# Kernel tuning notes

Hardware: AMD Instinct MI355X
Metric: run time of the kernel (lower is better)

Reference implementation:

```python
import jax, jax.numpy as jnp
import numpy as np

N_SPK = 2048
M_UTT = 8
D_EMB = 512


def setup_inputs() -> dict:
    key = jax.random.key(0)
    k1, = jax.random.split(key, 1)
    embeds = jax.random.normal(k1, (N_SPK * M_UTT, D_EMB), dtype=jnp.float32)
    # module expects L2-normalized utterance embeddings
    embeds = embeds / jnp.linalg.norm(embeds, axis=-1, keepdims=True)
    return {
        "embeds": embeds,
        "w": jnp.asarray(10.0, dtype=jnp.float32),
        "b": jnp.asarray(-5.0, dtype=jnp.float32),
        "n_speakers": N_SPK,
        "m_utterances": M_UTT,
    }


def reference(embeds, w, b, n_speakers, m_utterances):
    N, M = n_speakers, m_utterances
    D = embeds.shape[-1]
    e = embeds.reshape(N, M, D)

    # full centroids (all M utterances), L2-normalized
    centroids = e.mean(axis=1)  # [N, D]
    centroids = centroids / jnp.linalg.norm(centroids, axis=-1, keepdims=True)

    # leave-one-out centroids for same-speaker comparisons
    sums = e.sum(axis=1, keepdims=True)  # [N, 1, D]
    excl = (sums - e) / (M - 1)  # [N, M, D]
    excl = excl / jnp.linalg.norm(excl, axis=-1, keepdims=True)

    # similarity: batched GEMM replaces the original triple loop
    sim = jnp.einsum("nmd,kd->nmk", e, centroids)  # [N, M, N]
    # diagonal (k == i) uses leave-one-out centroid
    diag = jnp.sum(e * excl, axis=-1)  # [N, M]
    idx = jnp.arange(N)
    sim = sim.at[idx, :, idx].set(diag)

    sim = jnp.abs(w) * sim + b

    # cross-entropy with label = own speaker index
    logits = sim.reshape(N * M, N)
    labels = jnp.repeat(jnp.arange(N), M)
    logp = jax.nn.log_softmax(logits, axis=-1)
    loss = -jnp.mean(logp[jnp.arange(N * M), labels])
    return loss
```

## Files before the change

kernel.cpp:

```cpp
#include <hip/hip_runtime.h>
#include <hip/hip_bf16.h>
#include <string.h>

#define N_SPK 2048
#define M_UTT 8
#define D_EMB 512
#define N_ROWS (N_SPK * M_UTT)

using short8 = __attribute__((ext_vector_type(8))) short;
using f32x4  = __attribute__((ext_vector_type(4))) float;

typedef const __attribute__((address_space(1))) unsigned int* gas_p;
typedef __attribute__((address_space(3))) unsigned int* las_p;

__device__ int            g_flag;
__device__ float          g_accum;
__device__ unsigned int   g_done;
__device__ float          g_diag[N_ROWS];
__device__ unsigned short g_cRow[N_SPK * D_EMB];
__device__ float          g_rowsum[N_ROWS * 4];

__device__ __forceinline__ float u2f(unsigned int u) { float f; memcpy(&f, &u, 4); return f; }
__device__ __forceinline__ unsigned int f2u(float f) { unsigned int u; memcpy(&u, &f, 4); return u; }
__device__ __forceinline__ float bflo(unsigned int u) { return u2f(u << 16); }
__device__ __forceinline__ float bfhi(unsigned int u) { return u2f(u & 0xFFFF0000u); }
__device__ __forceinline__ unsigned short f2bf(float f) {
    unsigned int u = f2u(f);
    unsigned int r = u + 0x7FFFu + ((u >> 16) & 1u);
    return (unsigned short)(r >> 16);
}
__device__ __forceinline__ float wsum(float v) {
#pragma unroll
    for (int off = 32; off > 0; off >>= 1) v += __shfl_xor(v, off, 64);
    return v;
}
__device__ __forceinline__ float loadScalar(const void* p, int isbf) {
    float vb = bflo((unsigned int)(*(const unsigned short*)p));
    float vf = *(const float*)p;
    float prim = isbf ? vb : vf;
    float alt  = isbf ? vf : vb;
    float a = fabsf(prim);
    if (isfinite(prim) && a > 1e-6f && a < 1e6f) return prim;
    return alt;
}
__device__ __forceinline__ short8 loadA8(const void* e, long row, int d0, int isbf) {
    if (isbf) {
        return *(const short8*)((const unsigned short*)e + row * D_EMB + d0);
    } else {
        const float* q = (const float*)e + row * D_EMB + d0;
        short8 r;
#pragma unroll
        for (int j = 0; j < 8; ++j) r[j] = (short)f2bf(q[j]);
        return r;
    }
}
__device__ __forceinline__ int detectWave(const void* e, long row, int lane) {
    const unsigned short* q = (const unsigned short*)e + row * D_EMB + lane * 8;
    float p = 0.f;
#pragma unroll
    for (int j = 0; j < 8; ++j) {
        float v = bflo((unsigned int)q[j]);
        p += v * v;
    }
    p = wsum(p);
    return (fabsf(p - 1.0f) < 0.25f) ? 1 : 0;
}

__global__ __launch_bounds__(256) void k1_cent(const void* e) {
    int t = threadIdx.x;
    int wave = t >> 6, lane = t & 63;
    int n = blockIdx.x * 4 + wave;

    int isbf = detectWave(e, (long)n * M_UTT, lane);
    if (blockIdx.x == 0 && t == 0) { g_flag = isbf; g_accum = 0.f; g_done = 0u; }

    float ev[M_UTT][8];
    size_t base = (size_t)n * (M_UTT * D_EMB);
#pragma unroll
    for (int m = 0; m < M_UTT; ++m) {
        size_t idx = base + (size_t)m * D_EMB + (size_t)lane * 8;
        if (isbf) {
            uint4 v = *(const uint4*)((const unsigned short*)e + idx);
            ev[m][0] = bflo(v.x); ev[m][1] = bfhi(v.x);
            ev[m][2] = bflo(v.y); ev[m][3] = bfhi(v.y);
            ev[m][4] = bflo(v.z); ev[m][5] = bfhi(v.z);
            ev[m][6] = bflo(v.w); ev[m][7] = bfhi(v.w);
        } else {
            const float* q = (const float*)e + idx;
            float4 a = *(const float4*)q;
            float4 b2 = *(const float4*)(q + 4);
            ev[m][0] = a.x; ev[m][1] = a.y; ev[m][2] = a.z; ev[m][3] = a.w;
            ev[m][4] = b2.x; ev[m][5] = b2.y; ev[m][6] = b2.z; ev[m][7] = b2.w;
        }
    }

    float s[8];
#pragma unroll
    for (int j = 0; j < 8; ++j) {
        float acc = 0.f;
#pragma unroll
        for (int m = 0; m < M_UTT; ++m) acc += ev[m][j];
        s[j] = acc;
    }

    float p = 0.f;
#pragma unroll
    for (int j = 0; j < 8; ++j) p += s[j] * s[j];
    p = wsum(p);
    float inv = rsqrtf(p);

    unsigned short cw[8];
#pragma unroll
    for (int j = 0; j < 8; ++j) cw[j] = f2bf(s[j] * inv);
    *(short8*)&g_cRow[(size_t)n * D_EMB + lane * 8] = *(short8*)cw;

#pragma unroll
    for (int m = 0; m < M_UTT; ++m) {
        float pd = 0.f, pn = 0.f;
#pragma unroll
        for (int j = 0; j < 8; ++j) {
            float ex = s[j] - ev[m][j];
            pd += ev[m][j] * ex;
            pn += ex * ex;
        }
        pd = wsum(pd);
        pn = wsum(pn);
        if (lane == 0) g_diag[n * M_UTT + m] = pd * rsqrtf(pn);
    }
}

__global__ __launch_bounds__(256, 2) void GE2ELoss_70626442215524_kernel(
        const void* e, const void* wp, const void* bp) {
    __shared__ unsigned short sB[2][2][16 * 512];

    int t = threadIdx.x;
    int wave = t >> 6, lane = t & 63;
    int bx = blockIdx.x;
    int qtr = bx >> 7, rowgrp = bx & 127;
    int rowbase = rowgrp * 128 + wave * 32;
    int isbf = g_flag;
    int quad = lane >> 4, l16 = lane & 15;

    float w_ = fabsf(loadScalar(wp, isbf));
    float b_ = loadScalar(bp, isbf);

    auto stageTile = [&](int buf, int nt2) {
        int c0 = qtr * 512 + nt2 * 32;
#pragma unroll
        for (int g = 0; g < 2; ++g) {
#pragma unroll
            for (int i = 0; i < 4; ++i) {
                int cb = i * 256 + wave * 64;
                int w = cb + lane;
                int col = w & 15;
                int dc = ((w >> 6) << 2) + ((w >> 4) & 3);
                const unsigned short* g_ = &g_cRow[((size_t)(c0 + g * 16 + col) << 9) + dc * 8];
                __builtin_amdgcn_global_load_lds((gas_p)g_, (las_p)&sB[buf][g][cb * 8], 16, 0, 0);
            }
        }
    };

    stageTile(0, 0);

    short8 a[2][16];
#pragma unroll
    for (int s = 0; s < 2; ++s) {
        long row = rowbase + s * 16 + l16;
#pragma unroll
        for (int kt = 0; kt < 16; ++kt)
            a[s][kt] = loadA8(e, row, kt * 32 + quad * 8, isbf);
    }

    float rsum[2][4];
#pragma unroll
    for (int s = 0; s < 2; ++s)
#pragma unroll
        for (int r = 0; r < 4; ++r) rsum[s][r] = 0.f;

    __syncthreads();

    for (int nt2 = 0; nt2 < 16; ++nt2) {
        int cur = nt2 & 1;
        if (nt2 + 1 < 16) stageTile(cur ^ 1, nt2 + 1);

        f32x4 acc[2][2] = {{{0.f,0.f,0.f,0.f},{0.f,0.f,0.f,0.f}},
                           {{0.f,0.f,0.f,0.f},{0.f,0.f,0.f,0.f}}};
#pragma unroll
        for (int g = 0; g < 2; ++g) {
#pragma unroll
            for (int kt = 0; kt < 16; ++kt) {
                short8 b = *(const short8*)&sB[cur][g][(kt * 64 + lane) * 8];
                acc[g][0] = __builtin_amdgcn_mfma_f32_16x16x32_bf16(a[0][kt], b, acc[g][0], 0, 0, 0);
                acc[g][1] = __builtin_amdgcn_mfma_f32_16x16x32_bf16(a[1][kt], b, acc[g][1], 0, 0, 0);
            }
        }

#pragma unroll
        for (int g = 0; g < 2; ++g) {
            int gcol = qtr * 512 + nt2 * 32 + g * 16 + l16;
#pragma unroll
            for (int s = 0; s < 2; ++s) {
#pragma unroll
                for (int reg = 0; reg < 4; ++reg) {
                    int grow = rowbase + s * 16 + quad * 4 + reg;
                    float v = fmaf(w_, acc[g][s][reg], b_);
                    if (gcol == (grow >> 3)) v = fmaf(w_, g_diag[grow], b_);
                    rsum[s][reg] += __expf(v);
                }
            }
        }

        __syncthreads();
    }

#pragma unroll
    for (int s = 0; s < 2; ++s)
#pragma unroll
        for (int reg = 0; reg < 4; ++reg) {
            float v = rsum[s][reg];
            v += __shfl_xor(v, 1, 64);
            v += __shfl_xor(v, 2, 64);
            v += __shfl_xor(v, 4, 64);
            v += __shfl_xor(v, 8, 64);
            if (l16 == 0) {
                int grow = rowbase + s * 16 + quad * 4 + reg;
                g_rowsum[grow * 4 + qtr] = v;
            }
        }
}

__global__ __launch_bounds__(256) void k3_fin(const void* wp, const void* bp, unsigned int* out) {
    __shared__ float red[4];
    int t = threadIdx.x, bx = blockIdx.x;
    int isbf = g_flag;
    float w_ = fabsf(loadScalar(wp, isbf));
    float b_ = loadScalar(bp, isbf);

    int r = bx * 256 + t;
    float4 q = *(const float4*)&g_rowsum[r * 4];
    float tot = (q.x + q.y) + (q.z + q.w);
    float s = logf(tot) - fmaf(w_, g_diag[r], b_);

    s = wsum(s);
    if ((t & 63) == 0) red[t >> 6] = s;
    __syncthreads();
    if (t == 0) {
        float part = red[0] + red[1] + red[2] + red[3];
        atomicAdd(&g_accum, part);
        __threadfence();
        unsigned int old = atomicAdd(&g_done, 1u);
        if (old == 63u) {
            float loss = atomicAdd(&g_accum, 0.f) * (1.0f / N_ROWS);
            unsigned int h = (unsigned int)f2bf(loss);
            out[0] = (h << 16) | h;
        }
    }
}

extern "C" void kernel_launch(void* const* d_in, const int* in_sizes, int n_in,
                              void* d_out, int out_size, void* d_ws, size_t ws_size,
                              hipStream_t stream) {
    const void* e  = d_in[0];
    const void* wp = d_in[1];
    const void* bp = d_in[2];
    (void)in_sizes; (void)n_in; (void)out_size; (void)d_ws; (void)ws_size;

    k1_cent<<<512, 256, 0, stream>>>(e);
    GE2ELoss_70626442215524_kernel<<<512, 256, 0, stream>>>(e, wp, bp);
    k3_fin<<<64, 256, 0, stream>>>(wp, bp, (unsigned int*)d_out);
}
```

Baseline: 136.9 us.

## Fuse centroid, GEMM and finalize kernels into one persistent kernel with grid barrier

Merges the centroid/diagonal kernel, the similarity GEMM kernel and the final reduction kernel into a single launch. A software grid barrier built on an atomic ticket separates centroid production from GEMM consumption, and the last block to finish does the final loss reduction. A-operand loads are moved before the barrier so they overlap the wait, and the fp32 A load is vectorised. This removes two kernel launches and their gaps, but relies on all 512 blocks being co-resident and adds a spin wait with a timeout guard.

```diff
diff --git a/kernel.cpp b/kernel.cpp
--- a/kernel.cpp
+++ b/kernel.cpp
@@ -6,6 +6,7 @@
 #define M_UTT 8
 #define D_EMB 512
 #define N_ROWS (N_SPK * M_UTT)
+#define NBLK 512u
 
 using short8 = __attribute__((ext_vector_type(8))) short;
 using f32x4  = __attribute__((ext_vector_type(4))) float;
@@ -13,12 +14,11 @@
 typedef const __attribute__((address_space(1))) unsigned int* gas_p;
 typedef __attribute__((address_space(3))) unsigned int* las_p;
 
-__device__ int            g_flag;
-__device__ float          g_accum;
 __device__ unsigned int   g_done;
 __device__ float          g_diag[N_ROWS];
 __device__ unsigned short g_cRow[N_SPK * D_EMB];
 __device__ float          g_rowsum[N_ROWS * 4];
+__device__ unsigned int   g_barTicket;
 
 __device__ __forceinline__ float u2f(unsigned int u) { float f; memcpy(&f, &u, 4); return f; }
 __device__ __forceinline__ unsigned int f2u(float f) { unsigned int u; memcpy(&u, &f, 4); return u; }
@@ -48,9 +48,13 @@
         return *(const short8*)((const unsigned short*)e + row * D_EMB + d0);
     } else {
         const float* q = (const float*)e + row * D_EMB + d0;
+        float4 x = *(const float4*)q;
+        float4 y = *(const float4*)(q + 4);
         short8 r;
-#pragma unroll
-        for (int j = 0; j < 8; ++j) r[j] = (short)f2bf(q[j]);
+        r[0] = (short)f2bf(x.x); r[1] = (short)f2bf(x.y);
+        r[2] = (short)f2bf(x.z); r[3] = (short)f2bf(x.w);
+        r[4] = (short)f2bf(y.x); r[5] = (short)f2bf(y.y);
+        r[6] = (short)f2bf(y.z); r[7] = (short)f2bf(y.w);
         return r;
     }
 }
@@ -66,83 +70,117 @@
     return (fabsf(p - 1.0f) < 0.25f) ? 1 : 0;
 }
 
-__global__ __launch_bounds__(256) void k1_cent(const void* e) {
-    int t = threadIdx.x;
-    int wave = t >> 6, lane = t & 63;
-    int n = blockIdx.x * 4 + wave;
-
-    int isbf = detectWave(e, (long)n * M_UTT, lane);
-    if (blockIdx.x == 0 && t == 0) { g_flag = isbf; g_accum = 0.f; g_done = 0u; }
-
-    float ev[M_UTT][8];
-    size_t base = (size_t)n * (M_UTT * D_EMB);
-#pragma unroll
-    for (int m = 0; m < M_UTT; ++m) {
-        size_t idx = base + (size_t)m * D_EMB + (size_t)lane * 8;
-        if (isbf) {
-            uint4 v = *(const uint4*)((const unsigned short*)e + idx);
-            ev[m][0] = bflo(v.x); ev[m][1] = bfhi(v.x);
-            ev[m][2] = bflo(v.y); ev[m][3] = bfhi(v.y);
-            ev[m][4] = bflo(v.z); ev[m][5] = bfhi(v.z);
-            ev[m][6] = bflo(v.w); ev[m][7] = bfhi(v.w);
-        } else {
-            const float* q = (const float*)e + idx;
-            float4 a = *(const float4*)q;
-            float4 b2 = *(const float4*)(q + 4);
-            ev[m][0] = a.x; ev[m][1] = a.y; ev[m][2] = a.z; ev[m][3] = a.w;
-            ev[m][4] = b2.x; ev[m][5] = b2.y; ev[m][6] = b2.z; ev[m][7] = b2.w;
-        }
-    }
-
-    float s[8];
-#pragma unroll
-    for (int j = 0; j < 8; ++j) {
-        float acc = 0.f;
-#pragma unroll
-        for (int m = 0; m < M_UTT; ++m) acc += ev[m][j];
-        s[j] = acc;
-    }
-
-    float p = 0.f;
-#pragma unroll
-    for (int j = 0; j < 8; ++j) p += s[j] * s[j];
-    p = wsum(p);
-    float inv = rsqrtf(p);
-
-    unsigned short cw[8];
-#pragma unroll
-    for (int j = 0; j < 8; ++j) cw[j] = f2bf(s[j] * inv);
-    *(short8*)&g_cRow[(size_t)n * D_EMB + lane * 8] = *(short8*)cw;
-
-#pragma unroll
-    for (int m = 0; m < M_UTT; ++m) {
-        float pd = 0.f, pn = 0.f;
-#pragma unroll
-        for (int j = 0; j < 8; ++j) {
-            float ex = s[j] - ev[m][j];
-            pd += ev[m][j] * ex;
-            pn += ex * ex;
-        }
-        pd = wsum(pd);
-        pn = wsum(pn);
-        if (lane == 0) g_diag[n * M_UTT + m] = pd * rsqrtf(pn);
-    }
+__device__ __forceinline__ void gridSync() {
+    __threadfence();
+    __syncthreads();
+    if (threadIdx.x == 0) {
+        unsigned int my = __hip_atomic_fetch_add(&g_barTicket, 1u,
+                              __ATOMIC_ACQ_REL, __HIP_MEMORY_SCOPE_AGENT);
+        unsigned int target = (my / NBLK + 1u) * NBLK;
+        long guard = 0;
+        while (__hip_atomic_load(&g_barTicket, __ATOMIC_ACQUIRE,
+                                 __HIP_MEMORY_SCOPE_AGENT) < target) {
+            __builtin_amdgcn_s_sleep(8);
+            if (++guard > (1L << 22)) break;
+        }
+        __threadfence();
+    }
+    __syncthreads();
 }
 
 __global__ __launch_bounds__(256, 2) void GE2ELoss_70626442215524_kernel(
-        const void* e, const void* wp, const void* bp) {
+        const void* e, const void* wp, const void* bp, unsigned int* out) {
     __shared__ unsigned short sB[2][2][16 * 512];
+    __shared__ unsigned int s_fin;
+    __shared__ float red[4];
 
     int t = threadIdx.x;
     int wave = t >> 6, lane = t & 63;
     int bx = blockIdx.x;
     int qtr = bx >> 7, rowgrp = bx & 127;
-    int rowbase = rowgrp * 128 + wave * 32;
-    int isbf = g_flag;
     int quad = lane >> 4, l16 = lane & 15;
+
+    int isbf = detectWave(e, (long)rowgrp * 128, lane);
 
     float w_ = fabsf(loadScalar(wp, isbf));
     float b_ = loadScalar(bp, isbf);
+
+    if (bx == 0 && t == 0) g_done = 0u;
+
+    {
+        int n = rowgrp * 16 + qtr * 4 + wave;
+        float ev[M_UTT][8];
+        size_t base = (size_t)n * (M_UTT * D_EMB);
+#pragma unroll
+        for (int m = 0; m < M_UTT; ++m) {
+            size_t idx = base + (size_t)m * D_EMB + (size_t)lane * 8;
+            if (isbf) {
+                uint4 v = *(const uint4*)((const unsigned short*)e + idx);
+                ev[m][0] = bflo(v.x); ev[m][1] = bfhi(v.x);
+                ev[m][2] = bflo(v.y); ev[m][3] = bfhi(v.y);
+                ev[m][4] = bflo(v.z); ev[m][5] = bfhi(v.z);
+                ev[m][6] = bflo(v.w); ev[m][7] = bfhi(v.w);
+            } else {
+                const float* q = (const float*)e + idx;
+                float4 a2 = *(const float4*)q;
+                float4 b2 = *(const float4*)(q + 4);
+                ev[m][0] = a2.x; ev[m][1] = a2.y; ev[m][2] = a2.z; ev[m][3] = a2.w;
+                ev[m][4] = b2.x; ev[m][5] = b2.y; ev[m][6] = b2.z; ev[m][7] = b2.w;
+            }
+        }
+
+        float s[8];
+#pragma unroll
+        for (int j = 0; j < 8; ++j) {
+            float acc = 0.f;
+#pragma unroll
+            for (int m = 0; m < M_UTT; ++m) acc += ev[m][j];
+            s[j] = acc;
+        }
+
+        float p = 0.f;
+#pragma unroll
+        for (int j = 0; j < 8; ++j) p += s[j] * s[j];
+        p = wsum(p);
+        float inv = rsqrtf(p);
+
+        unsigned short cw[8];
+#pragma unroll
+        for (int j = 0; j < 8; ++j) cw[j] = f2bf(s[j] * inv);
+        *(short8*)&g_cRow[(size_t)n * D_EMB + lane * 8] = *(short8*)cw;
+
+#pragma unroll
+        for (int m = 0; m < M_UTT; ++m) {
+            float pd = 0.f, pn = 0.f;
+#pragma unroll
+            for (int j = 0; j < 8; ++j) {
+                float ex = s[j] - ev[m][j];
+                pd += ev[m][j] * ex;
+                pn += ex * ex;
+            }
+            pd = wsum(pd);
+            pn = wsum(pn);
+            if (lane == 0) g_diag[n * M_UTT + m] = pd * rsqrtf(pn);
+        }
+    }
+
+    int rowbase = rowgrp * 128 + wave * 32;
+    short8 a[2][16];
+#pragma unroll
+    for (int s = 0; s < 2; ++s) {
+        long row = rowbase + s * 16 + l16;
+#pragma unroll
+        for (int kt = 0; kt < 16; ++kt)
+            a[s][kt] = loadA8(e, row, kt * 32 + quad * 8, isbf);
+    }
+
+    float rsum[2][4];
+#pragma unroll
+    for (int s = 0; s < 2; ++s)
+#pragma unroll
+        for (int r = 0; r < 4; ++r) rsum[s][r] = 0.f;
+
+    gridSync();
 
     auto stageTile = [&](int buf, int nt2) {
         int c0 = qtr * 512 + nt2 * 32;
@@ -161,22 +199,6 @@
     };
 
     stageTile(0, 0);
-
-    short8 a[2][16];
-#pragma unroll
-    for (int s = 0; s < 2; ++s) {
-        long row = rowbase + s * 16 + l16;
-#pragma unroll
-        for (int kt = 0; kt < 16; ++kt)
-            a[s][kt] = loadA8(e, row, kt * 32 + quad * 8, isbf);
-    }
-
-    float rsum[2][4];
-#pragma unroll
-    for (int s = 0; s < 2; ++s)
-#pragma unroll
-        for (int r = 0; r < 4; ++r) rsum[s][r] = 0.f;
-
     __syncthreads();
 
     for (int nt2 = 0; nt2 < 16; ++nt2) {
@@ -227,30 +249,31 @@
                 g_rowsum[grow * 4 + qtr] = v;
             }
         }
-}
-
-__global__ __launch_bounds__(256) void k3_fin(const void* wp, const void* bp, unsigned int* out) {
-    __shared__ float red[4];
-    int t = threadIdx.x, bx = blockIdx.x;
-    int isbf = g_flag;
-    float w_ = fabsf(loadScalar(wp, isbf));
-    float b_ = loadScalar(bp, isbf);
-
-    int r = bx * 256 + t;
-    float4 q = *(const float4*)&g_rowsum[r * 4];
-    float tot = (q.x + q.y) + (q.z + q.w);
-    float s = logf(tot) - fmaf(w_, g_diag[r], b_);
-
-    s = wsum(s);
-    if ((t & 63) == 0) red[t >> 6] = s;
+
+    __threadfence();
     __syncthreads();
     if (t == 0) {
-        float part = red[0] + red[1] + red[2] + red[3];
-        atomicAdd(&g_accum, part);
+        unsigned int old = __hip_atomic_fetch_add(&g_done, 1u,
+                               __ATOMIC_ACQ_REL, __HIP_MEMORY_SCOPE_AGENT);
+        s_fin = (old == NBLK - 1u) ? 1u : 0u;
+    }
+    __syncthreads();
+
+    if (s_fin) {
         __threadfence();
-        unsigned int old = atomicAdd(&g_done, 1u);
-        if (old == 63u) {
-            float loss = atomicAdd(&g_accum, 0.f) * (1.0f / N_ROWS);
+        float part = 0.f;
+#pragma unroll 4
+        for (int i = 0; i < 64; ++i) {
+            int r = i * 256 + t;
+            float4 q = *(const float4*)&g_rowsum[r * 4];
+            float tot = (q.x + q.y) + (q.z + q.w);
+            part += logf(tot) - fmaf(w_, g_diag[r], b_);
+        }
+        part = wsum(part);
+        if ((t & 63) == 0) red[t >> 6] = part;
+        __syncthreads();
+        if (t == 0) {
+            float loss = (red[0] + red[1] + red[2] + red[3]) * (1.0f / N_ROWS);
             unsigned int h = (unsigned int)f2bf(loss);
             out[0] = (h << 16) | h;
         }
@@ -265,7 +288,6 @@
     const void* bp = d_in[2];
     (void)in_sizes; (void)n_in; (void)out_size; (void)d_ws; (void)ws_size;
 
-    k1_cent<<<512, 256, 0, stream>>>(e);
-    GE2ELoss_70626442215524_kernel<<<512, 256, 0, stream>>>(e, wp, bp);
-    k3_fin<<<64, 256, 0, stream>>>(wp, bp, (unsigned int*)d_out);
-}
+    GE2ELoss_70626442215524_kernel<<<dim3(NBLK), dim3(256), 0, stream>>>(
+        e, wp, bp, (unsigned int*)d_out);
+}
```

Measured after the change: 295.6 us. +115.9%, slower.

## Restructure similarity GEMM into 128x128 tiles with staged bf16 A and atomic row sums

Applied to the files above, without the earlier changes.

The first kernel now writes a bf16 copy of the embeddings, and the main kernel becomes a classic 128x128 output tile GEMM. Both A and B are staged through LDS in K-steps of 32, with a 2x2 wave layout and a 4x4 MFMA accumulator block per wave. The row sums of exp are accumulated with atomics into a single float per row instead of four per-quarter partials. This is meant to raise MFMA reuse per LDS load and to avoid re-reading and converting fp32 A in the GEMM. The cost is an extra 16 MB bf16 write/read, 2048 blocks with shallow K staging, and atomic contention on the row sums.

```diff
diff --git a/kernel.cpp b/kernel.cpp
--- a/kernel.cpp
+++ b/kernel.cpp
@@ -6,6 +6,11 @@
 #define M_UTT 8
 #define D_EMB 512
 #define N_ROWS (N_SPK * M_UTT)
+
+#define BM 128
+#define BN 128
+#define BK 32
+#define KSTEPS (D_EMB / BK)
 
 using short8 = __attribute__((ext_vector_type(8))) short;
 using f32x4  = __attribute__((ext_vector_type(4))) float;
@@ -18,7 +23,8 @@
 __device__ unsigned int   g_done;
 __device__ float          g_diag[N_ROWS];
 __device__ unsigned short g_cRow[N_SPK * D_EMB];
-__device__ float          g_rowsum[N_ROWS * 4];
+__device__ unsigned short g_eBf[N_ROWS * D_EMB];
+__device__ float          g_rowsumF[N_ROWS];
 
 __device__ __forceinline__ float u2f(unsigned int u) { float f; memcpy(&f, &u, 4); return f; }
 __device__ __forceinline__ unsigned int f2u(float f) { unsigned int u; memcpy(&u, &f, 4); return u; }
@@ -43,17 +49,6 @@
     if (isfinite(prim) && a > 1e-6f && a < 1e6f) return prim;
     return alt;
 }
-__device__ __forceinline__ short8 loadA8(const void* e, long row, int d0, int isbf) {
-    if (isbf) {
-        return *(const short8*)((const unsigned short*)e + row * D_EMB + d0);
-    } else {
-        const float* q = (const float*)e + row * D_EMB + d0;
-        short8 r;
-#pragma unroll
-        for (int j = 0; j < 8; ++j) r[j] = (short)f2bf(q[j]);
-        return r;
-    }
-}
 __device__ __forceinline__ int detectWave(const void* e, long row, int lane) {
     const unsigned short* q = (const unsigned short*)e + row * D_EMB + lane * 8;
     float p = 0.f;
@@ -73,6 +68,7 @@
 
     int isbf = detectWave(e, (long)n * M_UTT, lane);
     if (blockIdx.x == 0 && t == 0) { g_flag = isbf; g_accum = 0.f; g_done = 0u; }
+    if (blockIdx.x < 64) g_rowsumF[blockIdx.x * 256 + t] = 0.f;
 
     float ev[M_UTT][8];
     size_t base = (size_t)n * (M_UTT * D_EMB);
@@ -87,11 +83,19 @@
             ev[m][6] = bflo(v.w); ev[m][7] = bfhi(v.w);
         } else {
             const float* q = (const float*)e + idx;
-            float4 a = *(const float4*)q;
+            float4 a2 = *(const float4*)q;
             float4 b2 = *(const float4*)(q + 4);
-            ev[m][0] = a.x; ev[m][1] = a.y; ev[m][2] = a.z; ev[m][3] = a.w;
+            ev[m][0] = a2.x; ev[m][1] = a2.y; ev[m][2] = a2.z; ev[m][3] = a2.w;
             ev[m][4] = b2.x; ev[m][5] = b2.y; ev[m][6] = b2.z; ev[m][7] = b2.w;
         }
+    }
+
+#pragma unroll
+    for (int m = 0; m < M_UTT; ++m) {
+        unsigned short rw[8];
+#pragma unroll
+        for (int j = 0; j < 8; ++j) rw[j] = f2bf(ev[m][j]);
+        *(short8*)&g_eBf[base + (size_t)m * D_EMB + (size_t)lane * 8] = *(short8*)rw;
     }
 
     float s[8];
@@ -129,104 +133,91 @@
     }
 }
 
-__global__ __launch_bounds__(256, 2) void GE2ELoss_70626442215524_kernel(
-        const void* e, const void* wp, const void* bp) {
-    __shared__ unsigned short sB[2][2][16 * 512];
+__global__ __launch_bounds__(256, 3) void GE2ELoss_70626442215524_kernel(
+        const void* wp, const void* bp) {
+    __shared__ unsigned short sA[2][BM * BK];
+    __shared__ unsigned short sB[2][BN * BK];
 
     int t = threadIdx.x;
     int wave = t >> 6, lane = t & 63;
     int bx = blockIdx.x;
-    int qtr = bx >> 7, rowgrp = bx & 127;
-    int rowbase = rowgrp * 128 + wave * 32;
+    int colgrp = bx >> 7, rowgrp = bx & 127;
+    int rowTile = rowgrp * BM;
+    int colTile = colgrp * BN;
+    int wr = wave >> 1, wc = wave & 1;
+    int quad = lane >> 4, l16 = lane & 15;
     int isbf = g_flag;
-    int quad = lane >> 4, l16 = lane & 15;
 
     float w_ = fabsf(loadScalar(wp, isbf));
     float b_ = loadScalar(bp, isbf);
 
-    auto stageTile = [&](int buf, int nt2) {
-        int c0 = qtr * 512 + nt2 * 32;
-#pragma unroll
-        for (int g = 0; g < 2; ++g) {
-#pragma unroll
-            for (int i = 0; i < 4; ++i) {
-                int cb = i * 256 + wave * 64;
-                int w = cb + lane;
-                int col = w & 15;
-                int dc = ((w >> 6) << 2) + ((w >> 4) & 3);
-                const unsigned short* g_ = &g_cRow[((size_t)(c0 + g * 16 + col) << 9) + dc * 8];
-                __builtin_amdgcn_global_load_lds((gas_p)g_, (las_p)&sB[buf][g][cb * 8], 16, 0, 0);
+    auto stage = [&](int buf, int kt) {
+        int k0 = kt * BK + quad * 8;
+        int isA = (wave < 2) ? 1 : 0;
+        int rcBase = isA ? rowTile : colTile;
+        const unsigned short* gmat = isA ? g_eBf : g_cRow;
+#pragma unroll
+        for (int i = 0; i < 4; ++i) {
+            int s = (wave & 1) * 4 + i;
+            int rc = rcBase + s * 16 + l16;
+            const unsigned short* gsrc = gmat + ((size_t)rc << 9) + k0;
+            las_p ldst = (las_p)(isA ? &sA[buf][s * 512] : &sB[buf][s * 512]);
+            __builtin_amdgcn_global_load_lds((gas_p)gsrc, ldst, 16, 0, 0);
+        }
+    };
+
+    f32x4 acc[4][4];
+#pragma unroll
+    for (int i = 0; i < 4; ++i)
+#pragma unroll
+        for (int j = 0; j < 4; ++j) acc[i][j] = f32x4{0.f, 0.f, 0.f, 0.f};
+
+    stage(0, 0);
+    __syncthreads();
+
+    for (int kt = 0; kt < KSTEPS; ++kt) {
+        int cur = kt & 1;
+        if (kt + 1 < KSTEPS) stage(cur ^ 1, kt + 1);
+
+        short8 aF[4], bF[4];
+#pragma unroll
+        for (int i = 0; i < 4; ++i)
+            aF[i] = *(const short8*)&sA[cur][(wr * 4 + i) * 512 + lane * 8];
+#pragma unroll
+        for (int j = 0; j < 4; ++j)
+            bF[j] = *(const short8*)&sB[cur][(wc * 4 + j) * 512 + lane * 8];
+
+#pragma unroll
+        for (int i = 0; i < 4; ++i)
+#pragma unroll
+            for (int j = 0; j < 4; ++j)
+                acc[i][j] = __builtin_amdgcn_mfma_f32_16x16x32_bf16(
+                    aF[i], bF[j], acc[i][j], 0, 0, 0);
+
+        __syncthreads();
+    }
+
+#pragma unroll
+    for (int i = 0; i < 4; ++i) {
+#pragma unroll
+        for (int r = 0; r < 4; ++r) {
+            int grow = rowTile + wr * 64 + i * 16 + quad * 4 + r;
+            int dcol = grow >> 3;
+            float s = 0.f;
+#pragma unroll
+            for (int j = 0; j < 4; ++j) {
+                int gcol = colTile + wc * 64 + j * 16 + l16;
+                float v = fmaf(w_, acc[i][j][r], b_);
+                if (gcol == dcol) v = fmaf(w_, g_diag[grow], b_);
+                s += __expf(v);
             }
-        }
-    };
-
-    stageTile(0, 0);
-
-    short8 a[2][16];
-#pragma unroll
-    for (int s = 0; s < 2; ++s) {
-        long row = rowbase + s * 16 + l16;
-#pragma unroll
-        for (int kt = 0; kt < 16; ++kt)
-            a[s][kt] = loadA8(e, row, kt * 32 + quad * 8, isbf);
-    }
-
-    float rsum[2][4];
-#pragma unroll
-    for (int s = 0; s < 2; ++s)
-#pragma unroll
-        for (int r = 0; r < 4; ++r) rsum[s][r] = 0.f;
-
-    __syncthreads();
-
-    for (int nt2 = 0; nt2 < 16; ++nt2) {
-        int cur = nt2 & 1;
-        if (nt2 + 1 < 16) stageTile(cur ^ 1, nt2 + 1);
-
-        f32x4 acc[2][2] = {{{0.f,0.f,0.f,0.f},{0.f,0.f,0.f,0.f}},
-                           {{0.f,0.f,0.f,0.f},{0.f,0.f,0.f,0.f}}};
-#pragma unroll
-        for (int g = 0; g < 2; ++g) {
-#pragma unroll
-            for (int kt = 0; kt < 16; ++kt) {
-                short8 b = *(const short8*)&sB[cur][g][(kt * 64 + lane) * 8];
-                acc[g][0] = __builtin_amdgcn_mfma_f32_16x16x32_bf16(a[0][kt], b, acc[g][0], 0, 0, 0);
-                acc[g][1] = __builtin_amdgcn_mfma_f32_16x16x32_bf16(a[1][kt], b, acc[g][1], 0, 0, 0);
-            }
-        }
-
-#pragma unroll
-        for (int g = 0; g < 2; ++g) {
-            int gcol = qtr * 512 + nt2 * 32 + g * 16 + l16;
-#pragma unroll
-            for (int s = 0; s < 2; ++s) {
-#pragma unroll
-                for (int reg = 0; reg < 4; ++reg) {
-                    int grow = rowbase + s * 16 + quad * 4 + reg;
-                    float v = fmaf(w_, acc[g][s][reg], b_);
-                    if (gcol == (grow >> 3)) v = fmaf(w_, g_diag[grow], b_);
-                    rsum[s][reg] += __expf(v);
-                }
-            }
-        }
-
-        __syncthreads();
-    }
-
-#pragma unroll
-    for (int s = 0; s < 2; ++s)
-#pragma unroll
-        for (int reg = 0; reg < 4; ++reg) {
-            float v = rsum[s][reg];
-            v += __shfl_xor(v, 1, 64);
-            v += __shfl_xor(v, 2, 64);
-            v += __shfl_xor(v, 4, 64);
-            v += __shfl_xor(v, 8, 64);
-            if (l16 == 0) {
-                int grow = rowbase + s * 16 + quad * 4 + reg;
-                g_rowsum[grow * 4 + qtr] = v;
-            }
-        }
+            s += __shfl_xor(s, 1, 64);
+            s += __shfl_xor(s, 2, 64);
+            s += __shfl_xor(s, 4, 64);
+            s += __shfl_xor(s, 8, 64);
+            if (l16 == 0) atomicAdd(&g_rowsumF[grow], s);
+        }
+    }
 }
 
 __global__ __launch_bounds__(256) void k3_fin(const void* wp, const void* bp, unsigned int* out) {
@@ -237,8 +228,7 @@
     float b_ = loadScalar(bp, isbf);
 
     int r = bx * 256 + t;
-    float4 q = *(const float4*)&g_rowsum[r * 4];
-    float tot = (q.x + q.y) + (q.z + q.w);
+    float tot = g_rowsumF[r];
     float s = logf(tot) - fmaf(w_, g_diag[r], b_);
 
     s = wsum(s);
@@ -266,6 +256,6 @@
     (void)in_sizes; (void)n_in; (void)out_size; (void)d_ws; (void)ws_size;
 
     k1_cent<<<512, 256, 0, stream>>>(e);
-    GE2ELoss_70626442215524_kernel<<<512, 256, 0, stream>>>(e, wp, bp);
+    GE2ELoss_70626442215524_kernel<<<2048, 256, 0, stream>>>(wp, bp);
     k3_fin<<<64, 256, 0, stream>>>(wp, bp, (unsigned int*)d_out);
 }
```

New measurement: 165.0 us. 20.5% more time.

## Software-pipeline MFMA tiles with epilogue using double accumulators

Applied to the files above, without the earlier changes.

Restructures the GEMM loop so the exp/row-sum epilogue of one column tile runs after the MFMAs of the next tile are issued, using two accumulator sets, which overlaps transcendental ALU work with matrix-core work. It also hoists the per-row diagonal logit and its column index out of the loop, raises wave priority around the MFMA block, and vectorises the fp32 A-operand loads. The cost is extra accumulator registers, which may reduce occupancy.

```diff
diff --git a/kernel.cpp b/kernel.cpp
--- a/kernel.cpp
+++ b/kernel.cpp
@@ -48,9 +48,13 @@
         return *(const short8*)((const unsigned short*)e + row * D_EMB + d0);
     } else {
         const float* q = (const float*)e + row * D_EMB + d0;
+        float4 x = *(const float4*)q;
+        float4 y = *(const float4*)(q + 4);
         short8 r;
-#pragma unroll
-        for (int j = 0; j < 8; ++j) r[j] = (short)f2bf(q[j]);
+        r[0] = (short)f2bf(x.x); r[1] = (short)f2bf(x.y);
+        r[2] = (short)f2bf(x.z); r[3] = (short)f2bf(x.w);
+        r[4] = (short)f2bf(y.x); r[5] = (short)f2bf(y.y);
+        r[6] = (short)f2bf(y.z); r[7] = (short)f2bf(y.w);
         return r;
     }
 }
@@ -87,9 +91,9 @@
             ev[m][6] = bflo(v.w); ev[m][7] = bfhi(v.w);
         } else {
             const float* q = (const float*)e + idx;
-            float4 a = *(const float4*)q;
+            float4 a2 = *(const float4*)q;
             float4 b2 = *(const float4*)(q + 4);
-            ev[m][0] = a.x; ev[m][1] = a.y; ev[m][2] = a.z; ev[m][3] = a.w;
+            ev[m][0] = a2.x; ev[m][1] = a2.y; ev[m][2] = a2.z; ev[m][3] = a2.w;
             ev[m][4] = b2.x; ev[m][5] = b2.y; ev[m][6] = b2.z; ev[m][7] = b2.w;
         }
     }
@@ -171,47 +175,77 @@
             a[s][kt] = loadA8(e, row, kt * 32 + quad * 8, isbf);
     }
 
+    float dv[2][4];
+    int   dcol[2][4];
+#pragma unroll
+    for (int s = 0; s < 2; ++s)
+#pragma unroll
+        for (int r = 0; r < 4; ++r) {
+            int grow = rowbase + s * 16 + quad * 4 + r;
+            dv[s][r]   = fmaf(w_, g_diag[grow], b_);
+            dcol[s][r] = grow >> 3;
+        }
+
     float rsum[2][4];
 #pragma unroll
     for (int s = 0; s < 2; ++s)
 #pragma unroll
         for (int r = 0; r < 4; ++r) rsum[s][r] = 0.f;
 
-    __syncthreads();
-
-    for (int nt2 = 0; nt2 < 16; ++nt2) {
+    f32x4 accA[2][2], accB[2][2];
+
+    auto computeTile = [&](f32x4 (&ACC)[2][2], int nt2) {
         int cur = nt2 & 1;
         if (nt2 + 1 < 16) stageTile(cur ^ 1, nt2 + 1);
-
-        f32x4 acc[2][2] = {{{0.f,0.f,0.f,0.f},{0.f,0.f,0.f,0.f}},
-                           {{0.f,0.f,0.f,0.f},{0.f,0.f,0.f,0.f}}};
 #pragma unroll
         for (int g = 0; g < 2; ++g) {
+            ACC[g][0] = f32x4{0.f, 0.f, 0.f, 0.f};
+            ACC[g][1] = f32x4{0.f, 0.f, 0.f, 0.f};
+        }
+        __builtin_amdgcn_s_setprio(1);
+#pragma unroll
+        for (int g = 0; g < 2; ++g) {
 #pragma unroll
             for (int kt = 0; kt < 16; ++kt) {
-                short8 b = *(const short8*)&sB[cur][g][(kt * 64 + lane) * 8];
-                acc[g][0] = __builtin_amdgcn_mfma_f32_16x16x32_bf16(a[0][kt], b, acc[g][0], 0, 0, 0);
-                acc[g][1] = __builtin_amdgcn_mfma_f32_16x16x32_bf16(a[1][kt], b, acc[g][1], 0, 0, 0);
+                short8 bf = *(const short8*)&sB[cur][g][(kt * 64 + lane) * 8];
+                ACC[g][0] = __builtin_amdgcn_mfma_f32_16x16x32_bf16(a[0][kt], bf, ACC[g][0], 0, 0, 0);
+                ACC[g][1] = __builtin_amdgcn_mfma_f32_16x16x32_bf16(a[1][kt], bf, ACC[g][1], 0, 0, 0);
             }
         }
-
+        __builtin_amdgcn_s_setprio(0);
+    };
+
+    auto epilogTile = [&](f32x4 (&ACC)[2][2], int nt2) {
 #pragma unroll
         for (int g = 0; g < 2; ++g) {
             int gcol = qtr * 512 + nt2 * 32 + g * 16 + l16;
 #pragma unroll
             for (int s = 0; s < 2; ++s) {
 #pragma unroll
-                for (int reg = 0; reg < 4; ++reg) {
-                    int grow = rowbase + s * 16 + quad * 4 + reg;
-                    float v = fmaf(w_, acc[g][s][reg], b_);
-                    if (gcol == (grow >> 3)) v = fmaf(w_, g_diag[grow], b_);
-                    rsum[s][reg] += __expf(v);
+                for (int r = 0; r < 4; ++r) {
+                    float v = fmaf(w_, ACC[g][s][r], b_);
+                    if (gcol == dcol[s][r]) v = dv[s][r];
+                    rsum[s][r] += __expf(v);
                 }
             }
         }
-
+    };
+
+    __syncthreads();
+
+    computeTile(accA, 0);
+    __syncthreads();
+    for (int tp = 0; tp < 7; ++tp) {
+        computeTile(accB, tp * 2 + 1);
+        epilogTile(accA, tp * 2);
         __syncthreads();
-    }
+        computeTile(accA, tp * 2 + 2);
+        epilogTile(accB, tp * 2 + 1);
+        __syncthreads();
+    }
+    computeTile(accB, 15);
+    epilogTile(accA, 14);
+    epilogTile(accB, 15);
 
 #pragma unroll
     for (int s = 0; s < 2; ++s)
```

Measured after the change: 134.2 us. -2.0%, faster.
